# Kernel tuning notes

Measured on AMD Instinct MI355X. Metric: run time of the kernel, lower is better.

Reference implementation:

```python
import jax, jax.numpy as jnp
import numpy as np

B, L, S, C, H = 2, 2048, 2048, 1024, 16
HD = C // H  # head_dim = 64


def setup_inputs() -> dict:
    key = jax.random.key(0)
    k0, k1, k2, k3, k4 = jax.random.split(key, 5)
    w_scale = 1.0 / np.sqrt(C).astype(np.float32)
    return {
        "x0": jax.random.normal(k0, (B, L, C), jnp.float32),
        "x1": jax.random.normal(k1, (B, S, C), jnp.float32),
        "Wqk": jax.random.normal(k2, (C, C), jnp.float32) * w_scale,
        "Wv": jax.random.normal(k3, (C, C), jnp.float32) * w_scale,
        "Wmerge": jax.random.normal(k4, (C, C), jnp.float32) * w_scale,
    }


def reference(x0, x1, Wqk, Wv, Wmerge):
    softmax_temp = HD ** -0.5
    scale = softmax_temp ** 0.5  # applied to both qk0 and qk1

    def split_heads(t):  # [B,N,C] -> [B,N,H,HD]
        return t.reshape(t.shape[0], t.shape[1], H, HD)

    # shared QK projection (same weight for both streams), torch Linear: y = x @ W^T
    qk0 = split_heads(x0 @ Wqk.T) * scale  # [B,L,H,HD]
    qk1 = split_heads(x1 @ Wqk.T) * scale  # [B,S,H,HD]
    v0 = split_heads(x0 @ Wv.T)            # [B,L,H,HD]
    v1 = split_heads(x1 @ Wv.T)            # [B,S,H,HD]

    # single similarity matrix reused for both softmax directions
    sim = jnp.einsum('blhd,bshd->bhls', qk0, qk1)  # [B,H,L,S]
    attn01 = jax.nn.softmax(sim, axis=-1)  # softmax over S (x0 attends x1)
    attn10 = jax.nn.softmax(sim, axis=-2)  # softmax over L (== softmax(sim^T, -1))

    o0 = jnp.einsum('bhls,bshd->blhd', attn01, v1).reshape(x0.shape[0], x0.shape[1], C)
    o1 = jnp.einsum('bhls,blhd->bshd', attn10, v0).reshape(x1.shape[0], x1.shape[1], C)

    return (o0 @ Wmerge.T, o1 @ Wmerge.T)
```

## Files before the change

### kernel.cpp

```cpp
#include <hip/hip_runtime.h>
#include <hip/hip_bf16.h>
#include <stdint.h>


typedef __attribute__((ext_vector_type(8))) short bf16x8;
typedef __attribute__((ext_vector_type(4))) float f32x4;
typedef __attribute__((ext_vector_type(16))) float f32x16;
typedef __attribute__((ext_vector_type(4))) unsigned int u32x4;
typedef __attribute__((ext_vector_type(2))) unsigned int u32x2;
typedef __bf16 bf16_2 __attribute__((ext_vector_type(2)));

typedef const __attribute__((address_space(1))) unsigned int gu32;
typedef __attribute__((address_space(3))) unsigned int lu32;

__device__ __forceinline__ unsigned short f2bf(float f) {
  unsigned int u = __builtin_bit_cast(unsigned int, f);
  u += 0x7fffu + ((u >> 16) & 1u);
  return (unsigned short)(u >> 16);
}

__device__ __forceinline__ unsigned int cvtpk(float lo, float hi_) {
  bf16_2 t = { (__bf16)lo, (__bf16)hi_ };
  return __builtin_bit_cast(unsigned int, t);
}

__device__ __forceinline__ unsigned short f2bf_hw(float f) {
  return __builtin_bit_cast(unsigned short, (__bf16)f);
}

__global__ void cvt_x(const float* __restrict__ x0, const float* __restrict__ x1,
                      unsigned short* __restrict__ dst) {
  const long NX = 4194304;
  int y = blockIdx.y;
  const float* src = y ? x1 : x0;
  long i = ((long)blockIdx.x * 256 + threadIdx.x) * 8;
  float4 a = *(const float4*)(src + i);
  float4 b = *(const float4*)(src + i + 4);
  union { unsigned short u[8]; bf16x8 v; } r;
  r.u[0] = f2bf(a.x); r.u[1] = f2bf(a.y); r.u[2] = f2bf(a.z); r.u[3] = f2bf(a.w);
  r.u[4] = f2bf(b.x); r.u[5] = f2bf(b.y); r.u[6] = f2bf(b.z); r.u[7] = f2bf(b.w);
  *(bf16x8*)(dst + y * NX + i) = r.v;
}

__global__ void cvt_w(const float* __restrict__ w0, const float* __restrict__ w1,
                      const float* __restrict__ w2, unsigned short* __restrict__ dst) {
  const long NW = 1048576;
  int y = blockIdx.y;
  const float* src = (y == 0) ? w0 : ((y == 1) ? w1 : w2);
  long i = ((long)blockIdx.x * 256 + threadIdx.x) * 8;
  float4 a = *(const float4*)(src + i);
  float4 b = *(const float4*)(src + i + 4);
  union { unsigned short u[8]; bf16x8 v; } r;
  r.u[0] = f2bf(a.x); r.u[1] = f2bf(a.y); r.u[2] = f2bf(a.z); r.u[3] = f2bf(a.w);
  r.u[4] = f2bf(b.x); r.u[5] = f2bf(b.y); r.u[6] = f2bf(b.z); r.u[7] = f2bf(b.w);
  *(bf16x8*)(dst + y * NW + i) = r.v;
}

template<int OUTF32>
__global__ __launch_bounds__(256, 2)
void gemm_bt(const unsigned short* __restrict__ A, const unsigned short* __restrict__ B,
             void* __restrict__ C, int M, int N, int K, float scale) {
  __shared__ unsigned short As[128 * 32];
  __shared__ unsigned short Bs[128 * 32];
  const int tid = threadIdx.x;
  const int lane = tid & 63, w = tid >> 6;
  const int il = lane & 15, g = lane >> 4;
  const int wr = w >> 1, wc = w & 1;
  const int bm = blockIdx.y * 128, bn = blockIdx.x * 128;
  f32x4 acc[4][4];
#pragma unroll
  for (int m = 0; m < 4; ++m)
#pragma unroll
    for (int n = 0; n < 4; ++n) acc[m][n] = (f32x4){0.f, 0.f, 0.f, 0.f};

  const int crow = lane >> 2, ccol = (lane & 3) * 8;
  const int ch0 = w * 2, ch1 = w * 2 + 1;
  const unsigned short* pa0 = A + (long)(bm + ch0 * 16 + crow) * K + ccol;
  const unsigned short* pa1 = A + (long)(bm + ch1 * 16 + crow) * K + ccol;
  const unsigned short* pb0 = B + (long)(bn + ch0 * 16 + crow) * K + ccol;
  const unsigned short* pb1 = B + (long)(bn + ch1 * 16 + crow) * K + ccol;

  for (int k0 = 0; k0 < K; k0 += 32) {
    __builtin_amdgcn_global_load_lds((gu32*)(pa0 + k0), (lu32*)(As + ch0 * 512), 16, 0, 0);
    __builtin_amdgcn_global_load_lds((gu32*)(pa1 + k0), (lu32*)(As + ch1 * 512), 16, 0, 0);
    __builtin_amdgcn_global_load_lds((gu32*)(pb0 + k0), (lu32*)(Bs + ch0 * 512), 16, 0, 0);
    __builtin_amdgcn_global_load_lds((gu32*)(pb1 + k0), (lu32*)(Bs + ch1 * 512), 16, 0, 0);
    __syncthreads();
    bf16x8 av[4], bv[4];
#pragma unroll
    for (int m = 0; m < 4; ++m)
      av[m] = *(const bf16x8*)(As + (wr * 64 + m * 16 + il) * 32 + g * 8);
#pragma unroll
    for (int n = 0; n < 4; ++n)
      bv[n] = *(const bf16x8*)(Bs + (wc * 64 + n * 16 + il) * 32 + g * 8);
#pragma unroll
    for (int m = 0; m < 4; ++m)
#pragma unroll
      for (int n = 0; n < 4; ++n)
        acc[m][n] = __builtin_amdgcn_mfma_f32_16x16x32_bf16(av[m], bv[n], acc[m][n], 0, 0, 0);
    __syncthreads();
  }

#pragma unroll
  for (int m = 0; m < 4; ++m) {
    long row0 = bm + wr * 64 + m * 16 + g * 4;
#pragma unroll
    for (int n = 0; n < 4; ++n) {
      long col = bn + wc * 64 + n * 16 + il;
#pragma unroll
      for (int r = 0; r < 4; ++r) {
        float v = acc[m][n][r] * scale;
        if (OUTF32) ((float*)C)[(row0 + r) * (long)N + col] = v;
        else        ((unsigned short*)C)[(row0 + r) * (long)N + col] = f2bf(v);
      }
    }
  }
}

__global__ __launch_bounds__(256, 2)
void gemm_qkv(const unsigned short* __restrict__ A, const unsigned short* __restrict__ B,
              unsigned short* __restrict__ C0, unsigned short* __restrict__ C1, float scale0) {
  __shared__ unsigned short As[128 * 32];
  __shared__ unsigned short Bs[128 * 32];
  const int K = 1024;
  const int tid = threadIdx.x;
  const int lane = tid & 63, w = tid >> 6;
  const int il = lane & 15, g = lane >> 4;
  const int wr = w >> 1, wc = w & 1;
  const int bm = blockIdx.y * 128, bnn = blockIdx.x * 128;
  f32x4 acc[4][4];
#pragma unroll
  for (int m = 0; m < 4; ++m)
#pragma unroll
    for (int n = 0; n < 4; ++n) acc[m][n] = (f32x4){0.f, 0.f, 0.f, 0.f};

  const int crow = lane >> 2, ccol = (lane & 3) * 8;
  const int ch0 = w * 2, ch1 = w * 2 + 1;
  const unsigned short* pa0 = A + (long)(bm + ch0 * 16 + crow) * K + ccol;
  const unsigned short* pa1 = A + (long)(bm + ch1 * 16 + crow) * K + ccol;
  const unsigned short* pb0 = B + (long)(bnn + ch0 * 16 + crow) * K + ccol;
  const unsigned short* pb1 = B + (long)(bnn + ch1 * 16 + crow) * K + ccol;

  for (int k0 = 0; k0 < K; k0 += 32) {
    __builtin_amdgcn_global_load_lds((gu32*)(pa0 + k0), (lu32*)(As + ch0 * 512), 16, 0, 0);
    __builtin_amdgcn_global_load_lds((gu32*)(pa1 + k0), (lu32*)(As + ch1 * 512), 16, 0, 0);
    __builtin_amdgcn_global_load_lds((gu32*)(pb0 + k0), (lu32*)(Bs + ch0 * 512), 16, 0, 0);
    __builtin_amdgcn_global_load_lds((gu32*)(pb1 + k0), (lu32*)(Bs + ch1 * 512), 16, 0, 0);
    __syncthreads();
    bf16x8 av[4], bv[4];
#pragma unroll
    for (int m = 0; m < 4; ++m)
      av[m] = *(const bf16x8*)(As + (wr * 64 + m * 16 + il) * 32 + g * 8);
#pragma unroll
    for (int n = 0; n < 4; ++n)
      bv[n] = *(const bf16x8*)(Bs + (wc * 64 + n * 16 + il) * 32 + g * 8);
#pragma unroll
    for (int m = 0; m < 4; ++m)
#pragma unroll
      for (int n = 0; n < 4; ++n)
        acc[m][n] = __builtin_amdgcn_mfma_f32_16x16x32_bf16(av[m], bv[n], acc[m][n], 0, 0, 0);
    __syncthreads();
  }

  unsigned short* C = (bnn < 1024) ? C0 : C1;
  const int bn = bnn & 1023;
  const float scale = (bnn < 1024) ? scale0 : 1.f;
#pragma unroll
  for (int m = 0; m < 4; ++m) {
    long row0 = bm + wr * 64 + m * 16 + g * 4;
#pragma unroll
    for (int n = 0; n < 4; ++n) {
      long col = bn + wc * 64 + n * 16 + il;
#pragma unroll
      for (int r = 0; r < 4; ++r)
        C[(row0 + r) * 1024 + col] = f2bf(acc[m][n][r] * scale);
    }
  }
}

__global__ void transpose_v(const unsigned short* __restrict__ v, unsigned short* __restrict__ vt) {
  __shared__ unsigned short t[64][72];
  int bid = blockIdx.x;
  int tr = bid & 127, tc = bid >> 7;
  int tid = threadIdx.x;
  int rr = tid >> 2, c0 = (tid & 3) * 16;
  const unsigned short* s = v + (long)(tr * 64 + rr) * 1024 + tc * 64 + c0;
  *(bf16x8*)&t[rr][c0]     = *(const bf16x8*)s;
  *(bf16x8*)&t[rr][c0 + 8] = *(const bf16x8*)(s + 8);
  __syncthreads();
  int d = tid >> 2, n0 = (tid & 3) * 16;
  union { unsigned short u[16]; bf16x8 vv[2]; } r;
#pragma unroll
  for (int i = 0; i < 16; ++i) r.u[i] = t[n0 + i][d];
  unsigned short* o = vt + ((long)((tr >> 5) * 16 + tc) * 64 + d) * 2048 + (tr & 31) * 64 + n0;
  *(bf16x8*)o       = r.vv[0];
  *(bf16x8*)(o + 8) = r.vv[1];
}

__global__ __launch_bounds__(256, 4)
void attn_kernel(const unsigned short* __restrict__ qk,
                 const unsigned short* __restrict__ vt,
                 unsigned short* __restrict__ o) {
  __shared__ unsigned short sK[2][4096];
  __shared__ unsigned short sV[2][4096];
  int bid = blockIdx.x;
  int lb = (bid & 7) * 128 + (bid >> 3);
  int tid = threadIdx.x;
  int w = tid >> 6, lane = tid & 63;
  int u = lb * 4 + w;
  int dir = u >> 11, bh = (u >> 6) & 31, qu = u & 63;
  int b = bh >> 4, h = bh & 15;
  int q = lane & 31, hi = lane >> 5;

  long qrow0 = (dir ? 4096L : 0L) + b * 2048L + (long)qu * 32L;
  long krow0 = (dir ? 0L : 4096L) + b * 2048L;
  int vs = dir ? b : 2 + b;
  long vrow0 = (long)(vs * 16 + h) * 64;

  const unsigned short* Qp = qk + (qrow0 + q) * 1024 + h * 64 + hi * 8;

  int srow = tid >> 3;
  int sc = ((tid & 7) * 8) ^ ((srow & 7) << 3);
  const unsigned short* kg = qk + (krow0 + srow) * 1024 + h * 64 + sc;
  const unsigned short* vg = vt + (vrow0 + srow) * 2048 + sc;
  const int wbase = w * 512;

#define STAGE(BUF, T)                                                                    \
  {                                                                                      \
    long jj = (long)(T) * 64;                                                            \
    __builtin_amdgcn_global_load_lds((gu32*)(kg + jj * 1024),        (lu32*)(sK[BUF] + wbase),        16, 0, 0); \
    __builtin_amdgcn_global_load_lds((gu32*)(kg + (jj + 32) * 1024), (lu32*)(sK[BUF] + wbase + 2048), 16, 0, 0); \
    __builtin_amdgcn_global_load_lds((gu32*)(vg + jj),               (lu32*)(sV[BUF] + wbase),        16, 0, 0); \
    __builtin_amdgcn_global_load_lds((gu32*)(vg + jj + 32 * 2048),   (lu32*)(sV[BUF] + wbase + 2048), 16, 0, 0); \
  }

  bf16x8 qf[4];
#pragma unroll
  for (int ds = 0; ds < 4; ++ds)
    qf[ds] = *(const bf16x8*)(Qp + ds * 16);

  f32x16 z16;
#pragma unroll
  for (int j = 0; j < 16; ++j) z16[j] = 0.f;
  f32x16 accO[2];
  accO[0] = z16; accO[1] = z16;
  f32x16 lsum = z16;
  const short oneb = (short)0x3F80;
  const bf16x8 ones = {oneb, oneb, oneb, oneb, oneb, oneb, oneb, oneb};

  STAGE(0, 0);
  __syncthreads();

#pragma unroll 1
  for (int t = 0; t < 32; ++t) {
    int cur = t & 1;
    if (t < 31) STAGE(cur ^ 1, t + 1);

    bf16x8 kf[8], vf[8];
    int cswz = (q & 7) << 3;
#pragma unroll
    for (int kb = 0; kb < 2; ++kb)
#pragma unroll
      for (int ds = 0; ds < 4; ++ds)
        kf[kb * 4 + ds] = *(const bf16x8*)(&sK[cur][(kb * 32 + q) * 64 + ((ds * 16 + hi * 8) ^ cswz)]);
#pragma unroll
    for (int ks = 0; ks < 4; ++ks)
#pragma unroll
      for (int dn = 0; dn < 2; ++dn)
        vf[ks * 2 + dn] = *(const bf16x8*)(&sV[cur][(dn * 32 + q) * 64 + ((ks * 16 + hi * 8) ^ cswz)]);

    f32x16 st0 = __builtin_amdgcn_mfma_f32_32x32x16_bf16(kf[0], qf[0], z16, 0, 0, 0);
    f32x16 st1 = __builtin_amdgcn_mfma_f32_32x32x16_bf16(kf[4], qf[0], z16, 0, 0, 0);
#pragma unroll
    for (int ds = 1; ds < 4; ++ds)
      st0 = __builtin_amdgcn_mfma_f32_32x32x16_bf16(kf[ds], qf[ds], st0, 0, 0, 0);
#pragma unroll
    for (int ds = 1; ds < 4; ++ds)
      st1 = __builtin_amdgcn_mfma_f32_32x32x16_bf16(kf[4 + ds], qf[ds], st1, 0, 0, 0);

#pragma unroll
    for (int j = 0; j < 16; ++j) {
      st0[j] = __builtin_amdgcn_exp2f(st0[j]);
      st1[j] = __builtin_amdgcn_exp2f(st1[j]);
    }

    bf16x8 pa[4];
#pragma unroll
    for (int ks = 0; ks < 4; ++ks) {
      int m0 = (ks & 1) * 8;
      unsigned int a0, a1, b0, b1;
      if (ks < 2) {
        a0 = cvtpk(st0[m0],     st0[m0 + 1]); a1 = cvtpk(st0[m0 + 2], st0[m0 + 3]);
        b0 = cvtpk(st0[m0 + 4], st0[m0 + 5]); b1 = cvtpk(st0[m0 + 6], st0[m0 + 7]);
      } else {
        a0 = cvtpk(st1[m0],     st1[m0 + 1]); a1 = cvtpk(st1[m0 + 2], st1[m0 + 3]);
        b0 = cvtpk(st1[m0 + 4], st1[m0 + 5]); b1 = cvtpk(st1[m0 + 6], st1[m0 + 7]);
      }
      u32x2 r0 = __builtin_amdgcn_permlane32_swap(a0, b0, false, false);
      u32x2 r1 = __builtin_amdgcn_permlane32_swap(a1, b1, false, false);
      u32x4 uu = {r0[0], r1[0], r0[1], r1[1]};
      pa[ks] = __builtin_bit_cast(bf16x8, uu);
    }
#pragma unroll
    for (int ks = 0; ks < 4; ++ks)
      lsum = __builtin_amdgcn_mfma_f32_32x32x16_bf16(pa[ks], ones, lsum, 0, 0, 0);
#pragma unroll
    for (int ks = 0; ks < 4; ++ks)
#pragma unroll
      for (int dn = 0; dn < 2; ++dn)
        accO[dn] = __builtin_amdgcn_mfma_f32_32x32x16_bf16(pa[ks], vf[ks * 2 + dn], accO[dn], 0, 0, 0);

    __syncthreads();
  }
#undef STAGE

#pragma unroll
  for (int r = 0; r < 16; ++r) {
    int row = (r & 3) + 8 * (r >> 2) + 4 * hi;
    float invr = 1.f / lsum[r];
    long orow = qrow0 + row;
#pragma unroll
    for (int dn = 0; dn < 2; ++dn)
      o[orow * 1024 + h * 64 + dn * 32 + q] = f2bf_hw(accO[dn][r] * invr);
  }
}

extern "C" void kernel_launch(void* const* d_in, const int* in_sizes, int n_in,
                              void* d_out, int out_size, void* d_ws, size_t ws_size,
                              hipStream_t stream) {
  const float* x0 = (const float*)d_in[0];
  const float* x1 = (const float*)d_in[1];
  const float* Wqk = (const float*)d_in[2];
  const float* Wv = (const float*)d_in[3];
  const float* Wm = (const float*)d_in[4];
  float* out = (float*)d_out;

  const long NX = 4194304;
  const long NW = 1048576;
  unsigned short* xb  = (unsigned short*)d_ws;
  unsigned short* wb  = xb + 2 * NX;
  unsigned short* qkb = wb + 3 * NW;
  unsigned short* vb  = qkb + 2 * NX;
  unsigned short* vtb = vb + 2 * NX;

  cvt_x<<<dim3(2048, 2), 256, 0, stream>>>(x0, x1, xb);
  cvt_w<<<dim3(512, 3), 256, 0, stream>>>(Wqk, Wv, Wm, wb);

  const float sqk = 0.35355339059327373f * 1.2011224087864498f;
  gemm_qkv<<<dim3(16, 64), 256, 0, stream>>>(xb, wb, qkb, vb, sqk);
  transpose_v<<<2048, 256, 0, stream>>>(vb, vtb);
  attn_kernel<<<1024, 256, 0, stream>>>(qkb, vtb, vb);
  gemm_bt<1><<<dim3(8, 64), 256, 0, stream>>>(vb, wb + 2 * NW, out, 8192, 1024, 1024, 1.f);
}
```

Before: 172.0 us.

## Fuse V transpose into QKV GEMM epilogue and raise MFMA wave priority

```diff
diff --git a/kernel.cpp b/kernel.cpp
--- a/kernel.cpp
+++ b/kernel.cpp
@@ -119,9 +119,10 @@
 
 __global__ __launch_bounds__(256, 2)
 void gemm_qkv(const unsigned short* __restrict__ A, const unsigned short* __restrict__ B,
-              unsigned short* __restrict__ C0, unsigned short* __restrict__ C1, float scale0) {
+              unsigned short* __restrict__ C0, unsigned short* __restrict__ vt, float scale0) {
   __shared__ unsigned short As[128 * 32];
   __shared__ unsigned short Bs[128 * 32];
+  __shared__ unsigned short T[128][136];
   const int K = 1024;
   const int tid = threadIdx.x;
   const int lane = tid & 63, w = tid >> 6;
@@ -162,39 +163,39 @@
     __syncthreads();
   }
 
-  unsigned short* C = (bnn < 1024) ? C0 : C1;
-  const int bn = bnn & 1023;
-  const float scale = (bnn < 1024) ? scale0 : 1.f;
-#pragma unroll
-  for (int m = 0; m < 4; ++m) {
-    long row0 = bm + wr * 64 + m * 16 + g * 4;
-#pragma unroll
-    for (int n = 0; n < 4; ++n) {
-      long col = bn + wc * 64 + n * 16 + il;
-#pragma unroll
-      for (int r = 0; r < 4; ++r)
-        C[(row0 + r) * 1024 + col] = f2bf(acc[m][n][r] * scale);
-    }
-  }
-}
-
-__global__ void transpose_v(const unsigned short* __restrict__ v, unsigned short* __restrict__ vt) {
-  __shared__ unsigned short t[64][72];
-  int bid = blockIdx.x;
-  int tr = bid & 127, tc = bid >> 7;
-  int tid = threadIdx.x;
-  int rr = tid >> 2, c0 = (tid & 3) * 16;
-  const unsigned short* s = v + (long)(tr * 64 + rr) * 1024 + tc * 64 + c0;
-  *(bf16x8*)&t[rr][c0]     = *(const bf16x8*)s;
-  *(bf16x8*)&t[rr][c0 + 8] = *(const bf16x8*)(s + 8);
-  __syncthreads();
-  int d = tid >> 2, n0 = (tid & 3) * 16;
-  union { unsigned short u[16]; bf16x8 vv[2]; } r;
-#pragma unroll
-  for (int i = 0; i < 16; ++i) r.u[i] = t[n0 + i][d];
-  unsigned short* o = vt + ((long)((tr >> 5) * 16 + tc) * 64 + d) * 2048 + (tr & 31) * 64 + n0;
-  *(bf16x8*)o       = r.vv[0];
-  *(bf16x8*)(o + 8) = r.vv[1];
+  if (bnn < 1024) {
+#pragma unroll
+    for (int m = 0; m < 4; ++m) {
+      long row0 = bm + wr * 64 + m * 16 + g * 4;
+#pragma unroll
+      for (int n = 0; n < 4; ++n) {
+        long col = bnn + wc * 64 + n * 16 + il;
+#pragma unroll
+        for (int r = 0; r < 4; ++r)
+          C0[(row0 + r) * 1024 + col] = f2bf(acc[m][n][r] * scale0);
+      }
+    }
+  } else {
+#pragma unroll
+    for (int m = 0; m < 4; ++m) {
+      int rl = wr * 64 + m * 16 + g * 4;
+#pragma unroll
+      for (int n = 0; n < 4; ++n) {
+        int cl = wc * 64 + n * 16 + il;
+        u32x2 pk = { cvtpk(acc[m][n][0], acc[m][n][1]), cvtpk(acc[m][n][2], acc[m][n][3]) };
+        *(u32x2*)&T[cl][rl] = pk;
+      }
+    }
+    __syncthreads();
+    int cl2 = tid & 127, half = tid >> 7;
+    int s = bm >> 11;
+    int h0 = (bnn - 1024) >> 6;
+    unsigned short* dst = vt + (((long)(s * 16 + h0 + (cl2 >> 6))) * 64 + (cl2 & 63)) * 2048
+                             + (bm & 2047) + half * 64;
+#pragma unroll
+    for (int j = 0; j < 8; ++j)
+      *(bf16x8*)(dst + j * 8) = *(const bf16x8*)&T[cl2][half * 64 + j * 8];
+  }
 }
 
 __global__ __launch_bounds__(256, 4)
@@ -269,6 +270,7 @@
       for (int dn = 0; dn < 2; ++dn)
         vf[ks * 2 + dn] = *(const bf16x8*)(&sV[cur][(dn * 32 + q) * 64 + ((ks * 16 + hi * 8) ^ cswz)]);
 
+    __builtin_amdgcn_s_setprio(1);
     f32x16 st0 = __builtin_amdgcn_mfma_f32_32x32x16_bf16(kf[0], qf[0], z16, 0, 0, 0);
     f32x16 st1 = __builtin_amdgcn_mfma_f32_32x32x16_bf16(kf[4], qf[0], z16, 0, 0, 0);
 #pragma unroll
@@ -277,6 +279,7 @@
 #pragma unroll
     for (int ds = 1; ds < 4; ++ds)
       st1 = __builtin_amdgcn_mfma_f32_32x32x16_bf16(kf[4 + ds], qf[ds], st1, 0, 0, 0);
+    __builtin_amdgcn_s_setprio(0);
 
 #pragma unroll
     for (int j = 0; j < 16; ++j) {
@@ -301,6 +304,7 @@
       u32x4 uu = {r0[0], r1[0], r0[1], r1[1]};
       pa[ks] = __builtin_bit_cast(bf16x8, uu);
     }
+    __builtin_amdgcn_s_setprio(1);
 #pragma unroll
     for (int ks = 0; ks < 4; ++ks)
       lsum = __builtin_amdgcn_mfma_f32_32x32x16_bf16(pa[ks], ones, lsum, 0, 0, 0);
@@ -309,6 +313,7 @@
 #pragma unroll
       for (int dn = 0; dn < 2; ++dn)
         accO[dn] = __builtin_amdgcn_mfma_f32_32x32x16_bf16(pa[ks], vf[ks * 2 + dn], accO[dn], 0, 0, 0);
+    __builtin_amdgcn_s_setprio(0);
 
     __syncthreads();
   }
@@ -347,8 +352,7 @@
   cvt_w<<<dim3(512, 3), 256, 0, stream>>>(Wqk, Wv, Wm, wb);
 
   const float sqk = 0.35355339059327373f * 1.2011224087864498f;
-  gemm_qkv<<<dim3(16, 64), 256, 0, stream>>>(xb, wb, qkb, vb, sqk);
-  transpose_v<<<2048, 256, 0, stream>>>(vb, vtb);
+  gemm_qkv<<<dim3(16, 64), 256, 0, stream>>>(xb, wb, qkb, vtb, sqk);
   attn_kernel<<<1024, 256, 0, stream>>>(qkb, vtb, vb);
   gemm_bt<1><<<dim3(8, 64), 256, 0, stream>>>(vb, wb + 2 * NW, out, 8192, 1024, 1024, 1.f);
 }
```

Measured after the change: 418.5 us. 2.43x slower.
